# Kernel tuning notes

Measured on AMD Instinct MI355X. Metric: run time of the kernel, lower is better.

The kernel has to match this reference:

```python
import jax, jax.numpy as jnp
import numpy as np

EPS = 1e-7
LN_EPS = 1e-6


def project(x):
    norm = jnp.maximum(jnp.linalg.norm(x, axis=-1, keepdims=True), EPS)
    max_norm = 1.0 - EPS
    return jnp.where(norm >= 1.0, x / norm * max_norm, x)


def mobius_add(x, y, c):
    x2 = jnp.sum(x * x, -1, keepdims=True)
    y2 = jnp.sum(y * y, -1, keepdims=True)
    xy = jnp.sum(x * y, -1, keepdims=True)
    num = (1 + 2 * c * xy + c * y2) * x + (1 - c * x2) * y
    den = 1 + 2 * c * xy + c * c * x2 * y2
    return project(num / jnp.maximum(den, EPS))


def logmap0(y, c):
    sqrt_c = jnp.maximum(jnp.sqrt(c), EPS)
    y_norm = jnp.linalg.norm(y, axis=-1, keepdims=True)
    safe = jnp.maximum(y_norm, EPS)
    mag = jnp.arctanh(jnp.minimum(y_norm, 1.0 - EPS)) / sqrt_c
    return jnp.where(y_norm < EPS, jnp.zeros_like(y), mag * (y / safe))


def expmap0(v, c):
    sqrt_c = jnp.maximum(jnp.sqrt(c), EPS)
    v_norm = jnp.linalg.norm(v, axis=-1, keepdims=True)
    safe = jnp.maximum(v_norm, EPS)
    mag = jnp.tanh(sqrt_c * safe) / sqrt_c
    return project(jnp.where(v_norm < EPS, jnp.zeros_like(v), mag * (v / safe)))


def poincare_dist(x, y, c):
    # x: [B,H,N,1,D], y: [B,H,N,W,D], c: [B,1,1,1,1] -> dist [B,H,N,W]
    sqrt_c = jnp.maximum(jnp.sqrt(c), EPS)
    add_norm = jnp.linalg.norm(mobius_add(-x, y, c), axis=-1)
    arg = jnp.minimum(sqrt_c.squeeze(-1) * add_norm, 1.0 - EPS)
    return 2.0 * jnp.arctanh(arg) / sqrt_c.squeeze(-1)


def sliding_windows(x, window):
    # x: [B,H,N,Dh] -> [B,H,N,window,Dh] of the last `window` keys per query (zero-padded)
    B, H, N, Dh = x.shape
    pad = jnp.zeros((B, H, window - 1, Dh), dtype=x.dtype)
    xp = jnp.concatenate([pad, x], axis=2)
    idx = jnp.arange(window)[None, :] + jnp.arange(N)[:, None]  # [N, W]
    return xp[:, :, idx, :]


def layer_norm(x, scale, bias):
    mu = jnp.mean(x, axis=-1, keepdims=True)
    var = jnp.mean(jnp.square(x - mu), axis=-1, keepdims=True)
    return (x - mu) * jax.lax.rsqrt(var + LN_EPS) * scale + bias


def setup_inputs() -> dict:
    key = jax.random.key(0)
    B, N, DIM, H = 2, 1024, 1024, 16
    Dh = DIM // H
    ks = jax.random.split(key, 16)
    s = 1.0 / np.sqrt(DIM)
    x = 0.01 * jax.random.normal(ks[0], (B, N, DIM), jnp.float32)  # well inside the ball
    # rotary angles: pos * inv_freq, shape [N, Dh//2]
    inv_freq = 1.0 / (10000.0 ** (np.arange(0, Dh // 2, dtype=np.float32) * 2.0 / Dh))
    freqs = jnp.asarray(np.arange(N, dtype=np.float32)[:, None] * inv_freq[None, :])
    c = 0.5 + 0.5 * jax.random.uniform(ks[1], (B,), jnp.float32)
    p = {
        'Wq': s * jax.random.normal(ks[2], (DIM, DIM), jnp.float32), 'bq': jnp.zeros((DIM,), jnp.float32),
        'Wk': s * jax.random.normal(ks[3], (DIM, DIM), jnp.float32), 'bk': jnp.zeros((DIM,), jnp.float32),
        'Wv': s * jax.random.normal(ks[4], (DIM, DIM), jnp.float32), 'bv': jnp.zeros((DIM,), jnp.float32),
        'Wo': s * jax.random.normal(ks[5], (DIM, DIM), jnp.float32), 'bo': jnp.zeros((DIM,), jnp.float32),
        'W1': s * jax.random.normal(ks[6], (DIM, 4 * DIM), jnp.float32), 'b1': jnp.zeros((4 * DIM,), jnp.float32),
        'W2': (1.0 / np.sqrt(4 * DIM)) * jax.random.normal(ks[7], (4 * DIM, DIM), jnp.float32), 'b2': jnp.zeros((DIM,), jnp.float32),
        'ln1_scale': jnp.ones((DIM,), jnp.float32), 'ln1_bias': jnp.zeros((DIM,), jnp.float32),
        'ln2_scale': jnp.ones((DIM,), jnp.float32), 'ln2_bias': jnp.zeros((DIM,), jnp.float32),
        'geo_scale': jnp.ones((H, 1, 1), jnp.float32),
    }
    return dict(x=x, freqs=freqs, c=c, **p)


def reference(x, freqs, c, Wq, bq, Wk, bk, Wv, bv, Wo, bo, W1, b1, W2, b2,
              ln1_scale, ln1_bias, ln2_scale, ln2_bias, geo_scale):
    WINDOW = 32
    B, N, DIM = x.shape
    H = geo_scale.shape[0]
    Dh = DIM // H
    c_ln = c.reshape(B, 1, 1)
    c_attn = c.reshape(B, 1, 1, 1)
    c_d = c.reshape(B, 1, 1, 1, 1)

    # tangent-space layer norm 1
    x_norm = expmap0(layer_norm(logmap0(x, c_ln), ln1_scale, ln1_bias), c_ln)
    x_tan = logmap0(x_norm, c_ln)

    q = (x_tan @ Wq + bq).reshape(B, N, H, Dh)
    k = (x_tan @ Wk + bk).reshape(B, N, H, Dh)
    v = (x_tan @ Wv + bv).reshape(B, N, H, Dh)

    # rotary embedding (real-arithmetic form of complex multiply)
    cos = jnp.cos(freqs).reshape(1, N, 1, Dh // 2)
    sin = jnp.sin(freqs).reshape(1, N, 1, Dh // 2)

    def rope(t):
        t_r, t_i = jnp.split(t, 2, -1)
        return jnp.concatenate([t_r * cos - t_i * sin, t_r * sin + t_i * cos], -1)

    q_hyp = expmap0(rope(q), c_attn)
    k_hyp = expmap0(rope(k), c_attn)

    q_t = q_hyp.transpose(0, 2, 1, 3)  # [B,H,N,Dh]
    k_t = k_hyp.transpose(0, 2, 1, 3)
    v_t = v.transpose(0, 2, 1, 3)

    k_w = sliding_windows(k_t, WINDOW)  # [B,H,N,W,Dh]
    v_w = sliding_windows(v_t, WINDOW)

    dist = poincare_dist(q_t[:, :, :, None, :], k_w, c_d)  # [B,H,N,W]
    attn = jax.nn.softmax(-geo_scale * dist, axis=-1)
    attn_out = jnp.einsum('bhnw,bhnwd->bhnd', attn, v_w).transpose(0, 2, 1, 3).reshape(B, N, DIM)

    attn_hyp = expmap0(attn_out @ Wo + bo, c_ln)
    x_att = mobius_add(x, attn_hyp, c_ln)

    # tangent-space layer norm 2 + hyperbolic FFN
    x_norm2 = expmap0(layer_norm(logmap0(x_att, c_ln), ln2_scale, ln2_bias), c_ln)
    t = logmap0(x_norm2, c_ln)
    ffn_tan = jax.nn.gelu(t @ W1 + b1) @ W2 + b2
    x_ffn = expmap0(ffn_tan, c_ln)
    return mobius_add(x_att, x_ffn, c_ln)
```

## Files before the change

kernel.cpp:

```cpp
#include <hip/hip_runtime.h>
#include <cmath>

static constexpr int SEQ = 1024;
static constexpr int DIM = 1024;
static constexpr int NH  = 16;
static constexpr int DH  = 64;
static constexpr int WB  = 2;
static constexpr int ROWS = WB * SEQ;
__device__ static constexpr double D_EPS = 1e-7;

typedef unsigned short ushort_t;
typedef __attribute__((ext_vector_type(8))) short short8v;
typedef __attribute__((ext_vector_type(4))) float float4v;

__device__ __forceinline__ uint32_t bf16_hi_bits(float f) {
  uint32_t u = __float_as_uint(f);
  return (u + 0x7fffu + ((u >> 16) & 1u)) >> 16;
}

__device__ __forceinline__ size_t tiled_addr(int row, int col, int Kld) {
  return ((size_t)(row >> 7) * (Kld >> 5) + (col >> 5)) * 4096
       + (size_t)((((row >> 4) & 7) << 9) + (((col >> 3) & 3) << 7) + ((row & 15) << 3) + (col & 7));
}
__device__ __forceinline__ void store_hl(ushort_t* __restrict__ hi, ushort_t* __restrict__ lo,
                                         size_t addr, float f) {
  const uint32_t hb = bf16_hi_bits(f);
  hi[addr] = (ushort_t)hb;
  lo[addr] = (ushort_t)bf16_hi_bits(f - __uint_as_float(hb << 16));
}

__device__ __forceinline__ double wsum64(double v) {
#pragma unroll
  for (int m = 32; m >= 1; m >>= 1) v += __shfl_xor(v, m, 64);
  return v;
}

__global__ __launch_bounds__(256) void conv_w_kernel(
    const float* __restrict__ W, ushort_t* __restrict__ hi, ushort_t* __restrict__ lo,
    int K, int N) {
  const int tid = blockIdx.x * 256 + threadIdx.x;
  const int n = tid % N;
  const int k0 = (tid / N) << 3;
  uint32_t hw[4], lw[4];
#pragma unroll
  for (int rp = 0; rp < 4; rp++) {
    uint32_t h2[2], l2[2];
#pragma unroll
    for (int e = 0; e < 2; e++) {
      const float f = W[(size_t)(k0 + rp * 2 + e) * N + n];
      const uint32_t hb = bf16_hi_bits(f);
      h2[e] = hb;
      l2[e] = bf16_hi_bits(f - __uint_as_float(hb << 16));
    }
    hw[rp] = h2[0] | (h2[1] << 16);
    lw[rp] = l2[0] | (l2[1] << 16);
  }
  const size_t addr = tiled_addr(n, k0, K);
  *(uint4*)&hi[addr] = *(uint4*)hw;
  *(uint4*)&lo[addr] = *(uint4*)lw;
}

__global__ __launch_bounds__(256) void ln_tan_kernel(
    const float* __restrict__ xin, const float* __restrict__ cb,
    const float* __restrict__ gamma, const float* __restrict__ beta,
    ushort_t* __restrict__ ohi, ushort_t* __restrict__ olo) {
  __shared__ double sh[2][4];
  const int row = blockIdx.x;
  const int b = row / SEQ;
  const float* xr = xin + (size_t)row * DIM;
  const int t = threadIdx.x;
  float xv[4];
  double s0 = 0.0, s1 = 0.0;
#pragma unroll
  for (int i = 0; i < 4; i++) {
    xv[i] = xr[t + 256 * i];
    s0 += (double)xv[i];
    s1 += (double)xv[i] * (double)xv[i];
  }
  s0 = wsum64(s0); s1 = wsum64(s1);
  const int wid = t >> 6, lane = t & 63;
  if (lane == 0) { sh[0][wid] = s0; sh[1][wid] = s1; }
  __syncthreads();
  s0 = sh[0][0] + sh[0][1] + sh[0][2] + sh[0][3];
  s1 = sh[1][0] + sh[1][1] + sh[1][2] + sh[1][3];

  const double cc  = (double)cb[b];
  const double sqc = fmax(sqrt(cc), D_EPS);
  const double xn  = sqrt(s1);
  double a = 0.0;
  if (xn >= D_EPS) a = atanh(fmin(xn, 1.0 - D_EPS)) / sqc / fmax(xn, D_EPS);
  const double mu   = a * s0 / (double)DIM;
  const double var  = a * a * s1 / (double)DIM - mu * mu;
  const double invs = 1.0 / sqrt(var + 1e-6);

  double tv[4]; double s2 = 0.0;
#pragma unroll
  for (int i = 0; i < 4; i++) {
    const int col = t + 256 * i;
    tv[i] = (a * (double)xv[i] - mu) * invs * (double)gamma[col] + (double)beta[col];
    s2 += tv[i] * tv[i];
  }
  s2 = wsum64(s2);
  __syncthreads();
  if (lane == 0) sh[0][wid] = s2;
  __syncthreads();
  s2 = sh[0][0] + sh[0][1] + sh[0][2] + sh[0][3];

  const double tn = sqrt(s2);
  double C = 0.0;
  if (tn >= D_EPS) {
    const double safe_t = fmax(tn, D_EPS);
    const double mag2 = tanh(sqc * safe_t) / sqc;
    const double en = mag2 * (tn / safe_t);
    const double pn = fmax(en, D_EPS);
    const double f  = (pn >= 1.0) ? (1.0 - D_EPS) / pn : 1.0;
    const double yn = en * f;
    if (yn >= D_EPS) {
      const double mag3 = atanh(fmin(yn, 1.0 - D_EPS)) / sqc;
      C = (mag2 / safe_t) * f * (mag3 / fmax(yn, D_EPS));
    }
  }
#pragma unroll
  for (int i = 0; i < 4; i++) {
    const int col = t + 256 * i;
    store_hl(ohi, olo, tiled_addr(row, col, DIM), (float)(tv[i] * C));
  }
}

__global__ __launch_bounds__(256) void expmobius_parts4_kernel(
    const float* __restrict__ xb,
    const float* __restrict__ p0, const float* __restrict__ p1,
    const float* __restrict__ p2, const float* __restrict__ p3,
    const float* __restrict__ bias, const float* __restrict__ cb,
    float* __restrict__ out) {
  __shared__ double sh[3][4];
  const int row = blockIdx.x;
  const int b = row / SEQ;
  const size_t ro = (size_t)row * DIM;
  const int t = threadIdx.x;
  float xv[4];
  double tv[4];
  double sx2 = 0.0, st2 = 0.0, sxt = 0.0;
#pragma unroll
  for (int i = 0; i < 4; i++) {
    const int col = t + 256 * i;
    xv[i] = xb[ro + col];
    tv[i] = (double)p0[ro + col] + (double)p1[ro + col] +
            (double)p2[ro + col] + (double)p3[ro + col] + (double)bias[col];
    sx2 += (double)xv[i] * (double)xv[i];
    st2 += tv[i] * tv[i];
    sxt += (double)xv[i] * tv[i];
  }
  sx2 = wsum64(sx2); st2 = wsum64(st2); sxt = wsum64(sxt);
  const int wid = t >> 6, lane = t & 63;
  if (lane == 0) { sh[0][wid] = sx2; sh[1][wid] = st2; sh[2][wid] = sxt; }
  __syncthreads();
  sx2 = sh[0][0] + sh[0][1] + sh[0][2] + sh[0][3];
  st2 = sh[1][0] + sh[1][1] + sh[1][2] + sh[1][3];
  sxt = sh[2][0] + sh[2][1] + sh[2][2] + sh[2][3];

  const double cc  = (double)cb[b];
  const double sqc = fmax(sqrt(cc), D_EPS);
  const double tn = sqrt(st2);
  double s = 0.0;
  if (tn >= D_EPS) {
    const double safe = fmax(tn, D_EPS);
    const double mag = tanh(sqc * safe) / sqc;
    const double en = mag * (tn / safe);
    const double pn = fmax(en, D_EPS);
    const double f  = (pn >= 1.0) ? (1.0 - D_EPS) / pn : 1.0;
    s = (mag / safe) * f;
  }
  const double x2 = sx2, y2 = s * s * st2, xy = s * sxt;
  const double P   = 1.0 + 2.0 * cc * xy + cc * y2;
  const double Q   = 1.0 - cc * x2;
  const double den = fmax(1.0 + 2.0 * cc * xy + cc * cc * x2 * y2, D_EPS);
  const double num2 = P * P * x2 + Q * Q * y2 + 2.0 * P * Q * xy;
  const double rn  = sqrt(fmax(num2, 0.0)) / den;
  const double pn2 = fmax(rn, D_EPS);
  const double pf  = (pn2 >= 1.0) ? (1.0 - D_EPS) / pn2 : 1.0;
  const double Pd = (P / den) * pf;
  const double Qd = (Q / den) * pf * s;
#pragma unroll
  for (int i = 0; i < 4; i++)
    out[ro + t + 256 * i] = (float)(Pd * (double)xv[i] + Qd * tv[i]);
}

__global__ __launch_bounds__(256) void rope_expmap_kernel(
    float* __restrict__ q, float* __restrict__ k,
    const float* __restrict__ freqs, const float* __restrict__ cb) {
  const int row = blockIdx.x;
  const int b = row / SEQ, n = row % SEQ;
  const int t = threadIdx.x;
  const int h = t >> 4, j = t & 15;
  const int p1 = j, p2 = j + 16;
  const double f1 = (double)freqs[n * (DH / 2) + p1];
  const double f2 = (double)freqs[n * (DH / 2) + p2];
  const double c1 = cos(f1), s1 = sin(f1);
  const double c2 = cos(f2), s2 = sin(f2);
  const double cc  = (double)cb[b];
  const double sqc = fmax(sqrt(cc), D_EPS);
  const size_t base = (size_t)row * DIM + (size_t)h * DH;
  float* arrs[2] = {q, k};
#pragma unroll
  for (int a = 0; a < 2; a++) {
    float* p = arrs[a] + base;
    const double xr1 = p[p1], xi1 = p[p1 + 32];
    const double xr2 = p[p2], xi2 = p[p2 + 32];
    const double r1 = xr1 * c1 - xi1 * s1, i1 = xr1 * s1 + xi1 * c1;
    const double r2 = xr2 * c2 - xi2 * s2, i2 = xr2 * s2 + xi2 * c2;
    double nrm2 = r1 * r1 + i1 * i1 + r2 * r2 + i2 * i2;
#pragma unroll
    for (int m = 8; m >= 1; m >>= 1) nrm2 += __shfl_xor(nrm2, m, 16);
    const double vn = sqrt(nrm2);
    double sc = 0.0;
    if (vn >= D_EPS) {
      const double safe = fmax(vn, D_EPS);
      const double mag = tanh(sqc * safe) / sqc;
      const double en = mag * (vn / safe);
      const double pn = fmax(en, D_EPS);
      const double f  = (pn >= 1.0) ? (1.0 - D_EPS) / pn : 1.0;
      sc = (mag / safe) * f;
    }
    p[p1] = (float)(r1 * sc); p[p1 + 32] = (float)(i1 * sc);
    p[p2] = (float)(r2 * sc); p[p2 + 32] = (float)(i2 * sc);
  }
}

__global__ __launch_bounds__(256) void attn_kernel(
    const float* __restrict__ qh, const float* __restrict__ kh,
    const float* __restrict__ v, const float* __restrict__ cb,
    const float* __restrict__ geo,
    ushort_t* __restrict__ ohi, ushort_t* __restrict__ olo) {
  __shared__ float qs[8][DH];
  const int g = threadIdx.x >> 5;
  const int w = threadIdx.x & 31;
  const int gid = blockIdx.x * 8 + g;
  const int n = gid & (SEQ - 1);
  const int bh = gid >> 10;
  const int h = bh & (NH - 1);
  const int b = bh >> 4;
  const int row = b * SEQ + n;
  const size_t qbase = (size_t)row * DIM + (size_t)h * DH;
  qs[g][w] = qh[qbase + w];
  qs[g][w + 32] = qh[qbase + w + 32];
  __syncthreads();

  const double cc  = (double)cb[b];
  const double sqc = fmax(sqrt(cc), D_EPS);
  double q2p = (double)qs[g][w] * qs[g][w] + (double)qs[g][w + 32] * qs[g][w + 32];
#pragma unroll
  for (int m = 16; m >= 1; m >>= 1) q2p += __shfl_xor(q2p, m, 32);
  const double a2 = q2p;

  const int msrc = n - 31 + w;
  double y2 = 0.0, qy = 0.0;
  if (msrc >= 0) {
    const float* kr = kh + ((size_t)(b * SEQ + msrc)) * DIM + (size_t)h * DH;
#pragma unroll 8
    for (int d = 0; d < DH; d++) {
      const double kv = (double)kr[d];
      y2 += kv * kv;
      qy += (double)qs[g][d] * kv;
    }
  }
  const double ay = -qy;
  const double P = 1.0 + 2.0 * cc * ay + cc * y2;
  const double Q = 1.0 - cc * a2;
  const double den = fmax(1.0 + 2.0 * cc * ay + cc * cc * a2 * y2, D_EPS);
  const double num2 = P * P * a2 + Q * Q * y2 + 2.0 * P * Q * ay;
  const double rn = sqrt(fmax(num2, 0.0)) / den;
  const double pn = fmax(rn, D_EPS);
  const double addn = (pn >= 1.0) ? (1.0 - D_EPS) * (rn / pn) : rn;
  const double arg = fmin(sqc * addn, 1.0 - D_EPS);
  const double dist = 2.0 * atanh(arg) / sqc;
  const double logit = -(double)geo[h] * dist;

  double mx = logit;
#pragma unroll
  for (int m = 16; m >= 1; m >>= 1) mx = fmax(mx, __shfl_xor(mx, m, 32));
  const double e = exp(logit - mx);
  double se = e;
#pragma unroll
  for (int m = 16; m >= 1; m >>= 1) se += __shfl_xor(se, m, 32);
  const double p = e / se;

  double acc1 = 0.0, acc2 = 0.0;
  for (int wp = 0; wp < 32; wp++) {
    const double pw = __shfl(p, wp, 32);
    const int mp = n - 31 + wp;
    if (mp >= 0) {
      const float* vr = v + ((size_t)(b * SEQ + mp)) * DIM + (size_t)h * DH;
      acc1 += pw * (double)vr[w];
      acc2 += pw * (double)vr[w + 32];
    }
  }
  const int col = h * DH + w;
  store_hl(ohi, olo, tiled_addr(row, col, DIM), (float)acc1);
  store_hl(ohi, olo, tiled_addr(row, col + 32, DIM), (float)acc2);
}

__device__ __forceinline__ float gelu_tanh(float x) {
  const float x3 = x * x * x;
  return 0.5f * x * (1.0f + tanhf(0.7978845608028654f * (x + 0.044715f * x3)));
}

template <int EPI>
__device__ __forceinline__ void mfma_gemm_body(
    const ushort_t* __restrict__ Ahi, const ushort_t* __restrict__ Alo, int Kld,
    const ushort_t* __restrict__ Bhi, const ushort_t* __restrict__ Blo, int KB,
    const float* __restrict__ bias, float* __restrict__ Cf,
    ushort_t* __restrict__ Chi, ushort_t* __restrict__ Clo, int KldOut,
    int N, int k0, int klen, int m0, int n0) {
  __shared__ __align__(16) short AsH[4096], AsL[4096], BsH[4096], BsL[4096];
  const int t = threadIdx.x;
  const int lane = t & 63, wave = t >> 6;
  const int wm = (wave >> 1) << 6, wn = (wave & 1) << 6;
  const size_t abase = (size_t)(m0 >> 7) * (Kld >> 5) * 4096;
  const size_t bbase = (size_t)(n0 >> 7) * (KB >> 5) * 4096;

  float4v acc[4][4];
#pragma unroll
  for (int i = 0; i < 4; i++)
#pragma unroll
    for (int j = 0; j < 4; j++) acc[i][j] = (float4v){0.f, 0.f, 0.f, 0.f};

  uint4 rah0, rah1, ral0, ral1, rbh0, rbh1, rbl0, rbl1;
  {
    const size_t at = abase + (size_t)(k0 >> 5) * 4096;
    const size_t bt = bbase + (size_t)(k0 >> 5) * 4096;
    rah0 = ((const uint4*)(Ahi + at))[t]; rah1 = ((const uint4*)(Ahi + at))[t + 256];
    ral0 = ((const uint4*)(Alo + at))[t]; ral1 = ((const uint4*)(Alo + at))[t + 256];
    rbh0 = ((const uint4*)(Bhi + bt))[t]; rbh1 = ((const uint4*)(Bhi + bt))[t + 256];
    rbl0 = ((const uint4*)(Blo + bt))[t]; rbl1 = ((const uint4*)(Blo + bt))[t + 256];
  }

  for (int kt = 0; kt < klen; kt += 32) {
    __syncthreads();
    ((uint4*)AsH)[t] = rah0; ((uint4*)AsH)[t + 256] = rah1;
    ((uint4*)AsL)[t] = ral0; ((uint4*)AsL)[t + 256] = ral1;
    ((uint4*)BsH)[t] = rbh0; ((uint4*)BsH)[t + 256] = rbh1;
    ((uint4*)BsL)[t] = rbl0; ((uint4*)BsL)[t + 256] = rbl1;
    __syncthreads();
    {
      const int ktn = (kt + 32 < klen) ? kt + 32 : kt;
      const size_t at = abase + (size_t)((k0 + ktn) >> 5) * 4096;
      const size_t bt = bbase + (size_t)((k0 + ktn) >> 5) * 4096;
      rah0 = ((const uint4*)(Ahi + at))[t]; rah1 = ((const uint4*)(Ahi + at))[t + 256];
      ral0 = ((const uint4*)(Alo + at))[t]; ral1 = ((const uint4*)(Alo + at))[t + 256];
      rbh0 = ((const uint4*)(Bhi + bt))[t]; rbh1 = ((const uint4*)(Bhi + bt))[t + 256];
      rbl0 = ((const uint4*)(Blo + bt))[t]; rbl1 = ((const uint4*)(Blo + bt))[t + 256];
    }
    short8v aH[4], aL[4];
    const int ams = wm >> 4;
#pragma unroll
    for (int im = 0; im < 4; im++) {
      aH[im] = *(const short8v*)&AsH[(((ams + im) << 6) + lane) << 3];
      aL[im] = *(const short8v*)&AsL[(((ams + im) << 6) + lane) << 3];
    }
    const int bns = wn >> 4;
#pragma unroll
    for (int in_ = 0; in_ < 4; in_++) {
      const short8v bH = *(const short8v*)&BsH[(((bns + in_) << 6) + lane) << 3];
      const short8v bL = *(const short8v*)&BsL[(((bns + in_) << 6) + lane) << 3];
#pragma unroll
      for (int im = 0; im < 4; im++) {
        acc[im][in_] = __builtin_amdgcn_mfma_f32_16x16x32_bf16(aH[im], bH, acc[im][in_], 0, 0, 0);
        acc[im][in_] = __builtin_amdgcn_mfma_f32_16x16x32_bf16(aH[im], bL, acc[im][in_], 0, 0, 0);
        acc[im][in_] = __builtin_amdgcn_mfma_f32_16x16x32_bf16(aL[im], bH, acc[im][in_], 0, 0, 0);
      }
    }
  }
  const int cq = lane >> 4, ci = lane & 15;
#pragma unroll
  for (int im = 0; im < 4; im++) {
    const int row = m0 + wm + im * 16 + cq * 4;
#pragma unroll
    for (int in_ = 0; in_ < 4; in_++) {
      const int col = n0 + wn + in_ * 16 + ci;
      if (EPI == 2) {
#pragma unroll
        for (int r = 0; r < 4; r++) Cf[(size_t)(row + r) * N + col] = acc[im][in_][r];
      } else if (EPI == 0) {
        const float bv_ = bias[col];
#pragma unroll
        for (int r = 0; r < 4; r++) Cf[(size_t)(row + r) * N + col] = acc[im][in_][r] + bv_;
      } else {
        const float bv_ = bias[col];
#pragma unroll
        for (int r = 0; r < 4; r++)
          store_hl(Chi, Clo, tiled_addr(row + r, col, KldOut),
                   gelu_tanh(acc[im][in_][r] + bv_));
      }
    }
  }
}

__global__ __launch_bounds__(256) void qkv_mfma(
    const ushort_t* __restrict__ Ahi, const ushort_t* __restrict__ Alo,
    const ushort_t* __restrict__ Whi, const ushort_t* __restrict__ Wlo,
    const float* __restrict__ bq, const float* __restrict__ bk, const float* __restrict__ bv,
    float* __restrict__ Cq, float* __restrict__ Ck, float* __restrict__ Cv) {
  const int which = blockIdx.x >> 3;
  const int n0 = (blockIdx.x & 7) << 7;
  const size_t woff = (size_t)which * (1u << 20);
  const float* bias = (which == 0) ? bq : (which == 1) ? bk : bv;
  float* C = (which == 0) ? Cq : (which == 1) ? Ck : Cv;
  mfma_gemm_body<0>(Ahi, Alo, DIM, Whi + woff, Wlo + woff, DIM, bias, C,
                    nullptr, nullptr, 0, DIM, 0, DIM, blockIdx.y << 7, n0);
}

__global__ __launch_bounds__(256) void ffn_up_mfma(
    const ushort_t* __restrict__ Ahi, const ushort_t* __restrict__ Alo,
    const ushort_t* __restrict__ W1hi, const ushort_t* __restrict__ W1lo,
    const float* __restrict__ b1, ushort_t* __restrict__ Hhi, ushort_t* __restrict__ Hlo) {
  mfma_gemm_body<1>(Ahi, Alo, DIM, W1hi, W1lo, DIM, b1, nullptr, Hhi, Hlo, 4 * DIM,
                    4 * DIM, 0, DIM, blockIdx.y << 7, blockIdx.x << 7);
}

__global__ __launch_bounds__(256) void gemm_splitk_mfma(
    const ushort_t* __restrict__ Ahi, const ushort_t* __restrict__ Alo, int Kld,
    const ushort_t* __restrict__ Bhi, const ushort_t* __restrict__ Blo, int KB,
    float* __restrict__ C0, float* __restrict__ C1,
    float* __restrict__ C2, float* __restrict__ C3, int N, int klen) {
  const int z = blockIdx.z;
  float* C = (z == 0) ? C0 : (z == 1) ? C1 : (z == 2) ? C2 : C3;
  mfma_gemm_body<2>(Ahi, Alo, Kld, Bhi, Blo, KB, nullptr, C, nullptr, nullptr, 0,
                    N, z * klen, klen, blockIdx.y << 7, blockIdx.x << 7);
}

extern "C" void kernel_launch(void* const* d_in, const int* in_sizes, int n_in,
                              void* d_out, int out_size, void* d_ws, size_t ws_size,
                              hipStream_t stream) {
  const float* x     = (const float*)d_in[0];
  const float* freqs = (const float*)d_in[1];
  const float* c     = (const float*)d_in[2];
  const float* Wq = (const float*)d_in[3];  const float* bq = (const float*)d_in[4];
  const float* Wk = (const float*)d_in[5];  const float* bk = (const float*)d_in[6];
  const float* Wv = (const float*)d_in[7];  const float* bv = (const float*)d_in[8];
  const float* Wo = (const float*)d_in[9];  const float* bo = (const float*)d_in[10];
  const float* W1 = (const float*)d_in[11]; const float* b1 = (const float*)d_in[12];
  const float* W2 = (const float*)d_in[13]; const float* b2 = (const float*)d_in[14];
  const float* g1 = (const float*)d_in[15]; const float* be1 = (const float*)d_in[16];
  const float* g2 = (const float*)d_in[17]; const float* be2 = (const float*)d_in[18];
  const float* geo = (const float*)d_in[19];
  float* out = (float*)d_out;
  float* ws = (float*)d_ws;

  const size_t SZ = (size_t)ROWS * DIM;
  const size_t PL = SZ;
  const uint32_t M1 = 1u << 20;
  auto us = [&](int i) { return (ushort_t*)(ws + (size_t)i * SZ); };

  ushort_t* xt_hi = us(0);           ushort_t* xt_lo = us(0) + PL;
  float* qb = ws + 1 * SZ; float* kb = ws + 2 * SZ; float* vb = ws + 3 * SZ;
  ushort_t* at_hi = us(4);           ushort_t* at_lo = us(4) + PL;
  ushort_t* qkvo_hi = us(5);         ushort_t* qkvo_lo = us(6);
  ushort_t* w1_hi = us(7);           ushort_t* w1_lo = us(8);
  ushort_t* w2_hi = us(5);           ushort_t* w2_lo = us(6);
  ushort_t* t2_hi = us(4);           ushort_t* t2_lo = us(4) + PL;
  ushort_t* h1_hi = us(0);           ushort_t* h1_lo = us(2);
  float* x_att = out;

  conv_w_kernel<<<512, 256, 0, stream>>>(Wq, qkvo_hi + 0 * M1, qkvo_lo + 0 * M1, DIM, DIM);
  conv_w_kernel<<<512, 256, 0, stream>>>(Wk, qkvo_hi + 1 * M1, qkvo_lo + 1 * M1, DIM, DIM);
  conv_w_kernel<<<512, 256, 0, stream>>>(Wv, qkvo_hi + 2 * M1, qkvo_lo + 2 * M1, DIM, DIM);
  conv_w_kernel<<<512, 256, 0, stream>>>(Wo, qkvo_hi + 3 * M1, qkvo_lo + 3 * M1, DIM, DIM);
  conv_w_kernel<<<2048, 256, 0, stream>>>(W1, w1_hi, w1_lo, DIM, 4 * DIM);
  ln_tan_kernel<<<ROWS, 256, 0, stream>>>(x, c, g1, be1, xt_hi, xt_lo);
  qkv_mfma<<<dim3(24, ROWS / 128), 256, 0, stream>>>(
      xt_hi, xt_lo, qkvo_hi, qkvo_lo, bq, bk, bv, qb, kb, vb);
  rope_expmap_kernel<<<ROWS, 256, 0, stream>>>(qb, kb, freqs, c);
  attn_kernel<<<WB * NH * SEQ / 8, 256, 0, stream>>>(qb, kb, vb, c, geo, at_hi, at_lo);
  gemm_splitk_mfma<<<dim3(DIM / 128, ROWS / 128, 4), 256, 0, stream>>>(
      at_hi, at_lo, DIM, qkvo_hi + 3 * M1, qkvo_lo + 3 * M1, DIM,
      ws + 0 * SZ, ws + 1 * SZ, ws + 2 * SZ, ws + 3 * SZ, DIM, DIM / 4);
  conv_w_kernel<<<2048, 256, 0, stream>>>(W2, w2_hi, w2_lo, 4 * DIM, DIM);
  expmobius_parts4_kernel<<<ROWS, 256, 0, stream>>>(
      x, ws + 0 * SZ, ws + 1 * SZ, ws + 2 * SZ, ws + 3 * SZ, bo, c, x_att);
  ln_tan_kernel<<<ROWS, 256, 0, stream>>>(x_att, c, g2, be2, t2_hi, t2_lo);
  ffn_up_mfma<<<dim3(4 * DIM / 128, ROWS / 128), 256, 0, stream>>>(
      t2_hi, t2_lo, w1_hi, w1_lo, b1, h1_hi, h1_lo);
  gemm_splitk_mfma<<<dim3(DIM / 128, ROWS / 128, 4), 256, 0, stream>>>(
      h1_hi, h1_lo, 4 * DIM, w2_hi, w2_lo, 4 * DIM,
      ws + 4 * SZ, ws + 7 * SZ, ws + 8 * SZ, ws + 9 * SZ, DIM, DIM);
  expmobius_parts4_kernel<<<ROWS, 256, 0, stream>>>(
      x_att, ws + 4 * SZ, ws + 7 * SZ, ws + 8 * SZ, ws + 9 * SZ, b2, c, out);
  (void)in_sizes; (void)n_in; (void)out_size; (void)ws_size;
}
```

Baseline: 430.6 us.

## Merge weight conversions, fuse mobius-add with layer norm, double GEMM K-tile

Five per-weight bf16 hi/lo conversion launches become one kernel that picks its weight by block index. The first residual mobius-add kernel now also runs the tangent-space layer norm chain on its output in registers, so the separate ln_tan pass and its reread of x_att go away. The shared MFMA GEMM body stages a K-tile of 64 instead of 32, doubling LDS per block to 64 KB and the register prefetch buffers. That halves the loop iterations and barriers but may lower occupancy.

Result: slower. 802.3 us (+86.3%).

```diff
diff --git a/kernel.cpp b/kernel.cpp
--- a/kernel.cpp
+++ b/kernel.cpp
@@ -35,10 +35,9 @@
   return v;
 }
 
-__global__ __launch_bounds__(256) void conv_w_kernel(
+__device__ __forceinline__ void conv_w_body(
     const float* __restrict__ W, ushort_t* __restrict__ hi, ushort_t* __restrict__ lo,
-    int K, int N) {
-  const int tid = blockIdx.x * 256 + threadIdx.x;
+    int K, int N, int tid) {
   const int n = tid % N;
   const int k0 = (tid / N) << 3;
   uint32_t hw[4], lw[4];
@@ -60,31 +59,49 @@
   *(uint4*)&lo[addr] = *(uint4*)lw;
 }
 
-__global__ __launch_bounds__(256) void ln_tan_kernel(
-    const float* __restrict__ xin, const float* __restrict__ cb,
+__global__ __launch_bounds__(256) void conv_all_kernel(
+    const float* __restrict__ Wq, const float* __restrict__ Wk,
+    const float* __restrict__ Wv, const float* __restrict__ Wo,
+    const float* __restrict__ W1,
+    ushort_t* __restrict__ qkvo_hi, ushort_t* __restrict__ qkvo_lo,
+    ushort_t* __restrict__ w1_hi, ushort_t* __restrict__ w1_lo) {
+  const int blk = blockIdx.x;
+  if (blk < 2048) {
+    const int which = blk >> 9;
+    const float* W = (which == 0) ? Wq : (which == 1) ? Wk : (which == 2) ? Wv : Wo;
+    const size_t off = (size_t)which << 20;
+    conv_w_body(W, qkvo_hi + off, qkvo_lo + off, DIM, DIM,
+                (blk & 511) * 256 + threadIdx.x);
+  } else {
+    conv_w_body(W1, w1_hi, w1_lo, DIM, 4 * DIM, (blk - 2048) * 256 + threadIdx.x);
+  }
+}
+
+__global__ __launch_bounds__(256) void conv_w_kernel(
+    const float* __restrict__ W, ushort_t* __restrict__ hi, ushort_t* __restrict__ lo,
+    int K, int N) {
+  conv_w_body(W, hi, lo, K, N, blockIdx.x * 256 + threadIdx.x);
+}
+
+__device__ __forceinline__ void ln_chain_body(
+    const float xv[4], int row, double cc,
     const float* __restrict__ gamma, const float* __restrict__ beta,
-    ushort_t* __restrict__ ohi, ushort_t* __restrict__ olo) {
-  __shared__ double sh[2][4];
-  const int row = blockIdx.x;
-  const int b = row / SEQ;
-  const float* xr = xin + (size_t)row * DIM;
-  const int t = threadIdx.x;
-  float xv[4];
+    ushort_t* __restrict__ ohi, ushort_t* __restrict__ olo,
+    double sh[3][4], int t) {
   double s0 = 0.0, s1 = 0.0;
 #pragma unroll
   for (int i = 0; i < 4; i++) {
-    xv[i] = xr[t + 256 * i];
     s0 += (double)xv[i];
     s1 += (double)xv[i] * (double)xv[i];
   }
   s0 = wsum64(s0); s1 = wsum64(s1);
   const int wid = t >> 6, lane = t & 63;
+  __syncthreads();
   if (lane == 0) { sh[0][wid] = s0; sh[1][wid] = s1; }
   __syncthreads();
   s0 = sh[0][0] + sh[0][1] + sh[0][2] + sh[0][3];
   s1 = sh[1][0] + sh[1][1] + sh[1][2] + sh[1][3];
 
-  const double cc  = (double)cb[b];
   const double sqc = fmax(sqrt(cc), D_EPS);
   const double xn  = sqrt(s1);
   double a = 0.0;
@@ -125,6 +142,46 @@
     const int col = t + 256 * i;
     store_hl(ohi, olo, tiled_addr(row, col, DIM), (float)(tv[i] * C));
   }
+}
+
+__global__ __launch_bounds__(256) void ln_tan_kernel(
+    const float* __restrict__ xin, const float* __restrict__ cb,
+    const float* __restrict__ gamma, const float* __restrict__ beta,
+    ushort_t* __restrict__ ohi, ushort_t* __restrict__ olo) {
+  __shared__ double sh[3][4];
+  const int row = blockIdx.x;
+  const int b = row / SEQ;
+  const float* xr = xin + (size_t)row * DIM;
+  const int t = threadIdx.x;
+  float xv[4];
+#pragma unroll
+  for (int i = 0; i < 4; i++) xv[i] = xr[t + 256 * i];
+  ln_chain_body(xv, row, (double)cb[b], gamma, beta, ohi, olo, sh, t);
+}
+
+__device__ __forceinline__ void mobius_coef(
+    double sx2, double st2, double sxt, double cc, double& Pd, double& Qd) {
+  const double sqc = fmax(sqrt(cc), D_EPS);
+  const double tn = sqrt(st2);
+  double s = 0.0;
+  if (tn >= D_EPS) {
+    const double safe = fmax(tn, D_EPS);
+    const double mag = tanh(sqc * safe) / sqc;
+    const double en = mag * (tn / safe);
+    const double pn = fmax(en, D_EPS);
+    const double f  = (pn >= 1.0) ? (1.0 - D_EPS) / pn : 1.0;
+    s = (mag / safe) * f;
+  }
+  const double x2 = sx2, y2 = s * s * st2, xy = s * sxt;
+  const double P   = 1.0 + 2.0 * cc * xy + cc * y2;
+  const double Q   = 1.0 - cc * x2;
+  const double den = fmax(1.0 + 2.0 * cc * xy + cc * cc * x2 * y2, D_EPS);
+  const double num2 = P * P * x2 + Q * Q * y2 + 2.0 * P * Q * xy;
+  const double rn  = sqrt(fmax(num2, 0.0)) / den;
+  const double pn2 = fmax(rn, D_EPS);
+  const double pf  = (pn2 >= 1.0) ? (1.0 - D_EPS) / pn2 : 1.0;
+  Pd = (P / den) * pf;
+  Qd = (Q / den) * pf * s;
 }
 
 __global__ __launch_bounds__(256) void expmobius_parts4_kernel(
@@ -158,32 +215,55 @@
   sx2 = sh[0][0] + sh[0][1] + sh[0][2] + sh[0][3];
   st2 = sh[1][0] + sh[1][1] + sh[1][2] + sh[1][3];
   sxt = sh[2][0] + sh[2][1] + sh[2][2] + sh[2][3];
-
-  const double cc  = (double)cb[b];
-  const double sqc = fmax(sqrt(cc), D_EPS);
-  const double tn = sqrt(st2);
-  double s = 0.0;
-  if (tn >= D_EPS) {
-    const double safe = fmax(tn, D_EPS);
-    const double mag = tanh(sqc * safe) / sqc;
-    const double en = mag * (tn / safe);
-    const double pn = fmax(en, D_EPS);
-    const double f  = (pn >= 1.0) ? (1.0 - D_EPS) / pn : 1.0;
-    s = (mag / safe) * f;
-  }
-  const double x2 = sx2, y2 = s * s * st2, xy = s * sxt;
-  const double P   = 1.0 + 2.0 * cc * xy + cc * y2;
-  const double Q   = 1.0 - cc * x2;
-  const double den = fmax(1.0 + 2.0 * cc * xy + cc * cc * x2 * y2, D_EPS);
-  const double num2 = P * P * x2 + Q * Q * y2 + 2.0 * P * Q * xy;
-  const double rn  = sqrt(fmax(num2, 0.0)) / den;
-  const double pn2 = fmax(rn, D_EPS);
-  const double pf  = (pn2 >= 1.0) ? (1.0 - D_EPS) / pn2 : 1.0;
-  const double Pd = (P / den) * pf;
-  const double Qd = (Q / den) * pf * s;
+  double Pd, Qd;
+  mobius_coef(sx2, st2, sxt, (double)cb[b], Pd, Qd);
 #pragma unroll
   for (int i = 0; i < 4; i++)
     out[ro + t + 256 * i] = (float)(Pd * (double)xv[i] + Qd * tv[i]);
+}
+
+__global__ __launch_bounds__(256) void expmobius_ln_kernel(
+    const float* __restrict__ xb,
+    const float* __restrict__ p0, const float* __restrict__ p1,
+    const float* __restrict__ p2, const float* __restrict__ p3,
+    const float* __restrict__ bias, const float* __restrict__ cb,
+    const float* __restrict__ gamma, const float* __restrict__ beta,
+    float* __restrict__ out, ushort_t* __restrict__ ohi, ushort_t* __restrict__ olo) {
+  __shared__ double sh[3][4];
+  const int row = blockIdx.x;
+  const int b = row / SEQ;
+  const size_t ro = (size_t)row * DIM;
+  const int t = threadIdx.x;
+  float xv[4];
+  double tv[4];
+  double sx2 = 0.0, st2 = 0.0, sxt = 0.0;
+#pragma unroll
+  for (int i = 0; i < 4; i++) {
+    const int col = t + 256 * i;
+    xv[i] = xb[ro + col];
+    tv[i] = (double)p0[ro + col] + (double)p1[ro + col] +
+            (double)p2[ro + col] + (double)p3[ro + col] + (double)bias[col];
+    sx2 += (double)xv[i] * (double)xv[i];
+    st2 += tv[i] * tv[i];
+    sxt += (double)xv[i] * tv[i];
+  }
+  sx2 = wsum64(sx2); st2 = wsum64(st2); sxt = wsum64(sxt);
+  const int wid = t >> 6, lane = t & 63;
+  if (lane == 0) { sh[0][wid] = sx2; sh[1][wid] = st2; sh[2][wid] = sxt; }
+  __syncthreads();
+  sx2 = sh[0][0] + sh[0][1] + sh[0][2] + sh[0][3];
+  st2 = sh[1][0] + sh[1][1] + sh[1][2] + sh[1][3];
+  sxt = sh[2][0] + sh[2][1] + sh[2][2] + sh[2][3];
+  const double cc = (double)cb[b];
+  double Pd, Qd;
+  mobius_coef(sx2, st2, sxt, cc, Pd, Qd);
+  float ov[4];
+#pragma unroll
+  for (int i = 0; i < 4; i++) {
+    ov[i] = (float)(Pd * (double)xv[i] + Qd * tv[i]);
+    out[ro + t + 256 * i] = ov[i];
+  }
+  ln_chain_body(ov, row, cc, gamma, beta, ohi, olo, sh, t);
 }
 
 __global__ __launch_bounds__(256) void rope_expmap_kernel(
@@ -312,7 +392,7 @@
     const float* __restrict__ bias, float* __restrict__ Cf,
     ushort_t* __restrict__ Chi, ushort_t* __restrict__ Clo, int KldOut,
     int N, int k0, int klen, int m0, int n0) {
-  __shared__ __align__(16) short AsH[4096], AsL[4096], BsH[4096], BsL[4096];
+  __shared__ __align__(16) ushort_t AsH[8192], AsL[8192], BsH[8192], BsL[8192];
   const int t = threadIdx.x;
   const int lane = t & 63, wave = t >> 6;
   const int wm = (wave >> 1) << 6, wn = (wave & 1) << 6;
@@ -325,49 +405,67 @@
 #pragma unroll
     for (int j = 0; j < 4; j++) acc[i][j] = (float4v){0.f, 0.f, 0.f, 0.f};
 
-  uint4 rah0, rah1, ral0, ral1, rbh0, rbh1, rbl0, rbl1;
+  uint4 ra_h[4], ra_l[4], rb_h[4], rb_l[4];
   {
     const size_t at = abase + (size_t)(k0 >> 5) * 4096;
     const size_t bt = bbase + (size_t)(k0 >> 5) * 4096;
-    rah0 = ((const uint4*)(Ahi + at))[t]; rah1 = ((const uint4*)(Ahi + at))[t + 256];
-    ral0 = ((const uint4*)(Alo + at))[t]; ral1 = ((const uint4*)(Alo + at))[t + 256];
-    rbh0 = ((const uint4*)(Bhi + bt))[t]; rbh1 = ((const uint4*)(Bhi + bt))[t + 256];
-    rbl0 = ((const uint4*)(Blo + bt))[t]; rbl1 = ((const uint4*)(Blo + bt))[t + 256];
-  }
-
-  for (int kt = 0; kt < klen; kt += 32) {
+#pragma unroll
+    for (int c = 0; c < 4; c++) {
+      const int idx = (c >> 1) * 512 + (c & 1) * 256 + t;
+      ra_h[c] = ((const uint4*)(Ahi + at))[idx];
+      ra_l[c] = ((const uint4*)(Alo + at))[idx];
+      rb_h[c] = ((const uint4*)(Bhi + bt))[idx];
+      rb_l[c] = ((const uint4*)(Blo + bt))[idx];
+    }
+  }
+
+  for (int kt = 0; kt < klen; kt += 64) {
     __syncthreads();
-    ((uint4*)AsH)[t] = rah0; ((uint4*)AsH)[t + 256] = rah1;
-    ((uint4*)AsL)[t] = ral0; ((uint4*)AsL)[t + 256] = ral1;
-    ((uint4*)BsH)[t] = rbh0; ((uint4*)BsH)[t + 256] = rbh1;
-    ((uint4*)BsL)[t] = rbl0; ((uint4*)BsL)[t + 256] = rbl1;
+#pragma unroll
+    for (int c = 0; c < 4; c++) {
+      const int idx = (c >> 1) * 512 + (c & 1) * 256 + t;
+      ((uint4*)AsH)[idx] = ra_h[c];
+      ((uint4*)AsL)[idx] = ra_l[c];
+      ((uint4*)BsH)[idx] = rb_h[c];
+      ((uint4*)BsL)[idx] = rb_l[c];
+    }
     __syncthreads();
     {
-      const int ktn = (kt + 32 < klen) ? kt + 32 : kt;
+      const int ktn = (kt + 64 < klen) ? kt + 64 : kt;
       const size_t at = abase + (size_t)((k0 + ktn) >> 5) * 4096;
       const size_t bt = bbase + (size_t)((k0 + ktn) >> 5) * 4096;
-      rah0 = ((const uint4*)(Ahi + at))[t]; rah1 = ((const uint4*)(Ahi + at))[t + 256];
-      ral0 = ((const uint4*)(Alo + at))[t]; ral1 = ((const uint4*)(Alo + at))[t + 256];
-      rbh0 = ((const uint4*)(Bhi + bt))[t]; rbh1 = ((const uint4*)(Bhi + bt))[t + 256];
-      rbl0 = ((const uint4*)(Blo + bt))[t]; rbl1 = ((const uint4*)(Blo + bt))[t + 256];
-    }
-    short8v aH[4], aL[4];
-    const int ams = wm >> 4;
-#pragma unroll
-    for (int im = 0; im < 4; im++) {
-      aH[im] = *(const short8v*)&AsH[(((ams + im) << 6) + lane) << 3];
-      aL[im] = *(const short8v*)&AsL[(((ams + im) << 6) + lane) << 3];
-    }
-    const int bns = wn >> 4;
-#pragma unroll
-    for (int in_ = 0; in_ < 4; in_++) {
-      const short8v bH = *(const short8v*)&BsH[(((bns + in_) << 6) + lane) << 3];
-      const short8v bL = *(const short8v*)&BsL[(((bns + in_) << 6) + lane) << 3];
+#pragma unroll
+      for (int c = 0; c < 4; c++) {
+        const int idx = (c >> 1) * 512 + (c & 1) * 256 + t;
+        ra_h[c] = ((const uint4*)(Ahi + at))[idx];
+        ra_l[c] = ((const uint4*)(Alo + at))[idx];
+        rb_h[c] = ((const uint4*)(Bhi + bt))[idx];
+        rb_l[c] = ((const uint4*)(Blo + bt))[idx];
+      }
+    }
+#pragma unroll
+    for (int p = 0; p < 2; p++) {
+      const int pb = p << 12;
+      short8v aH[4], aL[4];
+      const int ams = wm >> 4;
 #pragma unroll
       for (int im = 0; im < 4; im++) {
-        acc[im][in_] = __builtin_amdgcn_mfma_f32_16x16x32_bf16(aH[im], bH, acc[im][in_], 0, 0, 0);
-        acc[im][in_] = __builtin_amdgcn_mfma_f32_16x16x32_bf16(aH[im], bL, acc[im][in_], 0, 0, 0);
-        acc[im][in_] = __builtin_amdgcn_mfma_f32_16x16x32_bf16(aL[im], bH, acc[im][in_], 0, 0, 0);
+        const int off = pb + ((((ams + im) << 6) + lane) << 3);
+        aH[im] = *(const short8v*)&AsH[off];
+        aL[im] = *(const short8v*)&AsL[off];
+      }
+      const int bns = wn >> 4;
+#pragma unroll
+      for (int in_ = 0; in_ < 4; in_++) {
+        const int off = pb + ((((bns + in_) << 6) + lane) << 3);
+        const short8v bH = *(const short8v*)&BsH[off];
+        const short8v bL = *(const short8v*)&BsL[off];
+#pragma unroll
+        for (int im = 0; im < 4; im++) {
+          acc[im][in_] = __builtin_amdgcn_mfma_f32_16x16x32_bf16(aH[im], bH, acc[im][in_], 0, 0, 0);
+          acc[im][in_] = __builtin_amdgcn_mfma_f32_16x16x32_bf16(aH[im], bL, acc[im][in_], 0, 0, 0);
+          acc[im][in_] = __builtin_amdgcn_mfma_f32_16x16x32_bf16(aL[im], bH, acc[im][in_], 0, 0, 0);
+        }
       }
     }
   }
@@ -403,7 +501,7 @@
     float* __restrict__ Cq, float* __restrict__ Ck, float* __restrict__ Cv) {
   const int which = blockIdx.x >> 3;
   const int n0 = (blockIdx.x & 7) << 7;
-  const size_t woff = (size_t)which * (1u << 20);
+  const size_t woff = (size_t)which << 20;
   const float* bias = (which == 0) ? bq : (which == 1) ? bk : bv;
   float* C = (which == 0) ? Cq : (which == 1) ? Ck : Cv;
   mfma_gemm_body<0>(Ahi, Alo, DIM, Whi + woff, Wlo + woff, DIM, bias, C,
@@ -462,11 +560,8 @@
   ushort_t* h1_hi = us(0);           ushort_t* h1_lo = us(2);
   float* x_att = out;
 
-  conv_w_kernel<<<512, 256, 0, stream>>>(Wq, qkvo_hi + 0 * M1, qkvo_lo + 0 * M1, DIM, DIM);
-  conv_w_kernel<<<512, 256, 0, stream>>>(Wk, qkvo_hi + 1 * M1, qkvo_lo + 1 * M1, DIM, DIM);
-  conv_w_kernel<<<512, 256, 0, stream>>>(Wv, qkvo_hi + 2 * M1, qkvo_lo + 2 * M1, DIM, DIM);
-  conv_w_kernel<<<512, 256, 0, stream>>>(Wo, qkvo_hi + 3 * M1, qkvo_lo + 3 * M1, DIM, DIM);
-  conv_w_kernel<<<2048, 256, 0, stream>>>(W1, w1_hi, w1_lo, DIM, 4 * DIM);
+  conv_all_kernel<<<4096, 256, 0, stream>>>(
+      Wq, Wk, Wv, Wo, W1, qkvo_hi, qkvo_lo, w1_hi, w1_lo);
   ln_tan_kernel<<<ROWS, 256, 0, stream>>>(x, c, g1, be1, xt_hi, xt_lo);
   qkv_mfma<<<dim3(24, ROWS / 128), 256, 0, stream>>>(
       xt_hi, xt_lo, qkvo_hi, qkvo_lo, bq, bk, bv, qb, kb, vb);
@@ -476,9 +571,9 @@
       at_hi, at_lo, DIM, qkvo_hi + 3 * M1, qkvo_lo + 3 * M1, DIM,
       ws + 0 * SZ, ws + 1 * SZ, ws + 2 * SZ, ws + 3 * SZ, DIM, DIM / 4);
   conv_w_kernel<<<2048, 256, 0, stream>>>(W2, w2_hi, w2_lo, 4 * DIM, DIM);
-  expmobius_parts4_kernel<<<ROWS, 256, 0, stream>>>(
-      x, ws + 0 * SZ, ws + 1 * SZ, ws + 2 * SZ, ws + 3 * SZ, bo, c, x_att);
-  ln_tan_kernel<<<ROWS, 256, 0, stream>>>(x_att, c, g2, be2, t2_hi, t2_lo);
+  expmobius_ln_kernel<<<ROWS, 256, 0, stream>>>(
+      x, ws + 0 * SZ, ws + 1 * SZ, ws + 2 * SZ, ws + 3 * SZ, bo, c,
+      g2, be2, x_att, t2_hi, t2_lo);
   ffn_up_mfma<<<dim3(4 * DIM / 128, ROWS / 128), 256, 0, stream>>>(
       t2_hi, t2_lo, w1_hi, w1_lo, b1, h1_hi, h1_lo);
   gemm_splitk_mfma<<<dim3(DIM / 128, ROWS / 128, 4), 256, 0, stream>>>(
```
